# Performance work log

Hardware: AMD Instinct MI355X
Metric: run time of the kernel (lower is better)

Reference implementation:

```python
import jax, jax.numpy as jnp
import numpy as np

BUCKETS = 256


def _gru_cell(x, h, W_ih, W_hh, b_ih, b_hh):
    # torch GRUCell math, gate order (r, z, n)
    gi = x @ W_ih.T + b_ih            # [B, 3H]
    gh = h @ W_hh.T + b_hh            # [B, 3H]
    i_r, i_z, i_n = jnp.split(gi, 3, axis=-1)
    h_r, h_z, h_n = jnp.split(gh, 3, axis=-1)
    r = jax.nn.sigmoid(i_r + h_r)
    z = jax.nn.sigmoid(i_z + h_z)
    n = jnp.tanh(i_n + r * h_n)
    return (1.0 - z) * n + z * h


def setup_inputs() -> dict:
    key = jax.random.key(0)
    ks = jax.random.split(key, 10)
    B, T, C, G, H, V = 16, 2000, 128, 512, 512, BUCKETS
    s = 0.1  # keep gates in a sane range
    return {
        "cond": jax.random.normal(ks[0], (B, T, C), jnp.float32),
        "h0": jnp.zeros((B, G), jnp.float32),
        "W_ih": jax.random.normal(ks[1], (3 * G, C), jnp.float32) * s,
        "W_hh": jax.random.normal(ks[2], (3 * G, G), jnp.float32) * s,
        "b_ih": jax.random.normal(ks[3], (3 * G,), jnp.float32) * s,
        "b_hh": jax.random.normal(ks[4], (3 * G,), jnp.float32) * s,
        "W_hid": jax.random.normal(ks[5], (H, G), jnp.float32) * s,
        "b_hid": jax.random.normal(ks[6], (H,), jnp.float32) * s,
        "W_out": jax.random.normal(ks[7], (V, H), jnp.float32) * s,
        "b_out": jax.random.normal(ks[8], (V,), jnp.float32) * s,
        "embedding": jax.random.normal(ks[9], (V, C), jnp.float32) * s,
    }


def reference(cond, h0, W_ih, W_hh, b_ih, b_hh, W_hid, b_hid, W_out, b_out, embedding):
    B, T, C = cond.shape
    keys = jax.random.split(jax.random.key(1), T)
    prev0 = jnp.full((B,), BUCKETS // 2, jnp.int32)  # mid-bucket = mu-law zero

    def step(carry, inp):
        h, prev = carry
        cond_t, k = inp
        x = cond_t + embedding[prev]                  # [B, C]
        h = _gru_cell(x, h, W_ih, W_hh, b_ih, b_hh)   # [B, G]
        hid = jax.nn.relu(h @ W_hid.T + b_hid)        # [B, H]
        logits = hid @ W_out.T + b_out                # [B, V]
        sample = jax.random.categorical(k, logits, axis=-1).astype(jnp.int32)
        return (h, sample), (logits, sample)

    (h_final, _), (logits, samples) = jax.lax.scan(
        step, (h0, prev0), (jnp.swapaxes(cond, 0, 1), keys))
    # logits: [T, B, V] -> [B, T, V]; samples: [T, B] -> [B, T]
    return jnp.swapaxes(logits, 0, 1), jnp.swapaxes(samples, 0, 1), h_final
```

## Files before the change

### kernel.cpp

```cpp
#include <hip/hip_runtime.h>
#include <stdint.h>
#include <math.h>

#define NBLK 128
#define NTHR 256
#define Bn 16
#define Tn 2000
#define Cn 128
#define Gn 512
#define Hn 512
#define Vn 256

#define WS_DBL_BASE 512
#define GRP_STRIDE  3072

#define OUT_SAMP ((size_t)Bn*Tn*Vn)
#define OUT_HF   (OUT_SAMP + (size_t)Bn*Tn)

__device__ __forceinline__ unsigned rotl32(unsigned v, int n) {
  return (v << n) | (v >> (32 - n));
}

__device__ __forceinline__ void threefry2x32(unsigned k0, unsigned k1,
                                             unsigned c0, unsigned c1,
                                             unsigned& o0, unsigned& o1) {
  unsigned ks2 = k0 ^ k1 ^ 0x1BD11BDAu;
  unsigned x0 = c0 + k0;
  unsigned x1 = c1 + k1;
#define TF_R(r) { x0 += x1; x1 = rotl32(x1, r); x1 ^= x0; }
  TF_R(13) TF_R(15) TF_R(26) TF_R(6)
  x0 += k1;  x1 += ks2 + 1u;
  TF_R(17) TF_R(29) TF_R(16) TF_R(24)
  x0 += ks2; x1 += k0 + 2u;
  TF_R(13) TF_R(15) TF_R(26) TF_R(6)
  x0 += k0;  x1 += k1 + 3u;
  TF_R(17) TF_R(29) TF_R(16) TF_R(24)
  x0 += k1;  x1 += ks2 + 4u;
  TF_R(13) TF_R(15) TF_R(26) TF_R(6)
  x0 += ks2; x1 += k0 + 5u;
#undef TF_R
  o0 = x0; o1 = x1;
}

__device__ __forceinline__ void st_bypass(double* p, double v) {
  __hip_atomic_store(p, v, __ATOMIC_RELAXED, __HIP_MEMORY_SCOPE_AGENT);
}
__device__ __forceinline__ double ld_bypass(const double* p) {
  return __hip_atomic_load(p, __ATOMIC_RELAXED, __HIP_MEMORY_SCOPE_AGENT);
}

__device__ __forceinline__ void gbar8(unsigned* flags, int slot, unsigned target) {
  asm volatile("s_waitcnt vmcnt(0)" ::: "memory");
  __syncthreads();
  if (threadIdx.x == 0)
    __hip_atomic_store(&flags[slot], target, __ATOMIC_RELAXED,
                       __HIP_MEMORY_SCOPE_AGENT);
  if (threadIdx.x < 8) {
    int guard = 0;
    while (__hip_atomic_load(&flags[threadIdx.x], __ATOMIC_RELAXED,
                             __HIP_MEMORY_SCOPE_AGENT) < target) {
      if (++guard > 5000000) break;
    }
  }
  asm volatile("" ::: "memory");
  __syncthreads();
}

extern "C" __global__ __launch_bounds__(NTHR)
void wavernn_groups(const float* __restrict__ cond, const float* __restrict__ h0,
                    const float* __restrict__ W_ih, const float* __restrict__ W_hh,
                    const float* __restrict__ b_ih, const float* __restrict__ b_hh,
                    const float* __restrict__ W_hid, const float* __restrict__ b_hid,
                    const float* __restrict__ W_out, const float* __restrict__ b_out,
                    const float* __restrict__ emb,
                    float* __restrict__ out, double* __restrict__ ws) {
  const int tid = threadIdx.x;
  const int blk = blockIdx.x;
  const int g = blk >> 3;
  const int j = blk & 7;

  unsigned* flags = ((unsigned*)ws) + (size_t)g * 64;
  double* G   = ws + WS_DBL_BASE + (size_t)g * GRP_STRIDE;
  double* Hb0 = G;
  double* Hb1 = G + 512;
  double* PL  = G + 1024;

  __shared__ __attribute__((aligned(32))) double s_x[Cn];
  __shared__ __attribute__((aligned(32))) double s_h[Gn];
  __shared__ __attribute__((aligned(32))) double s_hid[64];
  __shared__ double s_r[64], s_z[64], s_hn[64], s_in[64];
  __shared__ double s_part[64][4];
  __shared__ double s_red[NTHR];
  __shared__ int    s_idx[NTHR];

  if (tid < 64) st_bypass(&Hb0[j * 64 + tid],
                          (double)h0[(size_t)g * Gn + j * 64 + tid]);
  if (tid < Cn) s_x[tid] = (double)cond[(size_t)g * Tn * Cn + tid]
                         + (double)emb[128 * Cn + tid];
  unsigned pc = 1;
  gbar8(flags, j, pc++);

  for (int t = 0; t < Tn; ++t) {
    double* hcur = (t & 1) ? Hb1 : Hb0;
    double* hnxt = (t & 1) ? Hb0 : Hb1;

    s_h[tid] = ld_bypass(&hcur[tid]);
    s_h[tid + 256] = ld_bypass(&hcur[tid + 256]);
    __syncthreads();
    {
      const int part = tid >> 6, gl = tid & 63;
      const double4* x4 = (const double4*)s_x;
      const double4* h4 = (const double4*)s_h;
      if (part <= 1) {
        const int row = part * 512 + j * 64 + gl;
        const float4* wi = (const float4*)(W_ih + (size_t)row * Cn);
        const float4* wh = (const float4*)(W_hh + (size_t)row * Gn);
        double a0 = 0., a1 = 0., a2 = 0., a3 = 0.;
#pragma unroll 8
        for (int k = 0; k < Cn / 4; ++k) {
          float4 w = wi[k]; double4 xv = x4[k];
          a0 = fma((double)w.x, xv.x, a0); a1 = fma((double)w.y, xv.y, a1);
          a2 = fma((double)w.z, xv.z, a2); a3 = fma((double)w.w, xv.w, a3);
        }
#pragma unroll 8
        for (int k = 0; k < Gn / 4; ++k) {
          float4 w = wh[k]; double4 hv = h4[k];
          a0 = fma((double)w.x, hv.x, a0); a1 = fma((double)w.y, hv.y, a1);
          a2 = fma((double)w.z, hv.z, a2); a3 = fma((double)w.w, hv.w, a3);
        }
        double pre = ((a0 + a1) + (a2 + a3)) + (double)b_ih[row] + (double)b_hh[row];
        double sig = 1.0 / (1.0 + exp(-pre));
        if (part == 0) s_r[gl] = sig; else s_z[gl] = sig;
      } else if (part == 2) {
        const int row = 1024 + j * 64 + gl;
        const float4* wh = (const float4*)(W_hh + (size_t)row * Gn);
        double a0 = 0., a1 = 0., a2 = 0., a3 = 0.;
#pragma unroll 8
        for (int k = 0; k < Gn / 4; ++k) {
          float4 w = wh[k]; double4 hv = h4[k];
          a0 = fma((double)w.x, hv.x, a0); a1 = fma((double)w.y, hv.y, a1);
          a2 = fma((double)w.z, hv.z, a2); a3 = fma((double)w.w, hv.w, a3);
        }
        s_hn[gl] = ((a0 + a1) + (a2 + a3)) + (double)b_hh[row];
      } else {
        const int row = 1024 + j * 64 + gl;
        const float4* wi = (const float4*)(W_ih + (size_t)row * Cn);
        double a0 = 0., a1 = 0., a2 = 0., a3 = 0.;
#pragma unroll 8
        for (int k = 0; k < Cn / 4; ++k) {
          float4 w = wi[k]; double4 xv = x4[k];
          a0 = fma((double)w.x, xv.x, a0); a1 = fma((double)w.y, xv.y, a1);
          a2 = fma((double)w.z, xv.z, a2); a3 = fma((double)w.w, xv.w, a3);
        }
        s_in[gl] = ((a0 + a1) + (a2 + a3)) + (double)b_ih[row];
      }
    }
    __syncthreads();
    if (tid < 64) {
      double r = s_r[tid], z = s_z[tid];
      double n = tanh(s_in[tid] + r * s_hn[tid]);
      double hv = (1.0 - z) * n + z * s_h[j * 64 + tid];
      st_bypass(&hnxt[j * 64 + tid], hv);
    }
    gbar8(flags, j, pc++);

    float cond_next = 0.f;
    if (t + 1 < Tn && tid < Cn)
      cond_next = cond[((size_t)g * Tn + (t + 1)) * Cn + tid];

    s_h[tid] = ld_bypass(&hnxt[tid]);
    s_h[tid + 256] = ld_bypass(&hnxt[tid + 256]);
    __syncthreads();
    if (t == Tn - 1 && j == 0) {
      out[OUT_HF + (size_t)g * Gn + tid] = (float)s_h[tid];
      out[OUT_HF + (size_t)g * Gn + tid + 256] = (float)s_h[tid + 256];
    }
    {
      const int row = j * 64 + (tid >> 2);
      const int q = tid & 3;
      const float4* wr = (const float4*)(W_hid + (size_t)row * Gn + q * 128);
      const double4* hh = (const double4*)(s_h + q * 128);
      double a0 = 0., a1 = 0., a2 = 0., a3 = 0.;
#pragma unroll 8
      for (int k = 0; k < 32; ++k) {
        float4 w = wr[k]; double4 hv = hh[k];
        a0 = fma((double)w.x, hv.x, a0); a1 = fma((double)w.y, hv.y, a1);
        a2 = fma((double)w.z, hv.z, a2); a3 = fma((double)w.w, hv.w, a3);
      }
      s_part[tid >> 2][q] = (a0 + a1) + (a2 + a3);
    }
    __syncthreads();
    if (tid < 64) {
      double acc = (s_part[tid][0] + s_part[tid][1])
                 + (s_part[tid][2] + s_part[tid][3])
                 + (double)b_hid[j * 64 + tid];
      s_hid[tid] = acc > 0.0 ? acc : 0.0;
    }
    __syncthreads();
    {
      const int v = tid;
      const float4* wr = (const float4*)(W_out + (size_t)v * Hn + j * 64);
      const double4* hh = (const double4*)s_hid;
      double a0 = 0., a1 = 0., a2 = 0., a3 = 0.;
#pragma unroll 8
      for (int k = 0; k < 16; ++k) {
        float4 w = wr[k]; double4 hv = hh[k];
        a0 = fma((double)w.x, hv.x, a0); a1 = fma((double)w.y, hv.y, a1);
        a2 = fma((double)w.z, hv.z, a2); a3 = fma((double)w.w, hv.w, a3);
      }
      st_bypass(&PL[j * 256 + v], (a0 + a1) + (a2 + a3));
    }
    gbar8(flags, j, pc++);

    {
      const int v = tid;
      double l0 = ld_bypass(&PL[0 * 256 + v]);
      double l1 = ld_bypass(&PL[1 * 256 + v]);
      double l2 = ld_bypass(&PL[2 * 256 + v]);
      double l3 = ld_bypass(&PL[3 * 256 + v]);
      double l4 = ld_bypass(&PL[4 * 256 + v]);
      double l5 = ld_bypass(&PL[5 * 256 + v]);
      double l6 = ld_bypass(&PL[6 * 256 + v]);
      double l7 = ld_bypass(&PL[7 * 256 + v]);
      double logit = ((((((((l0 + l1) + l2) + l3) + l4) + l5) + l6) + l7))
                   + (double)b_out[v];
      if (j == 0)
        out[(size_t)g * Tn * Vn + (size_t)t * Vn + v] = (float)logit;

      unsigned kt0, kt1, r0, r1;
      threefry2x32(0u, 1u, 0u, (unsigned)t, kt0, kt1);
      threefry2x32(kt0, kt1, 0u, (unsigned)(g * Vn + v), r0, r1);
      unsigned bits = r0 ^ r1;
      float uf = __uint_as_float((bits >> 9) | 0x3f800000u) - 1.0f;
      if (uf <= 0.f) uf = 1.17549435e-38f;
      double gum = -log(-log((double)uf));
      s_red[tid] = logit + gum;
      s_idx[tid] = v;
    }
    __syncthreads();
    for (int s2 = NTHR / 2; s2 > 0; s2 >>= 1) {
      if (tid < s2) {
        double ov = s_red[tid + s2]; int oi = s_idx[tid + s2];
        if (ov > s_red[tid] || (ov == s_red[tid] && oi < s_idx[tid])) {
          s_red[tid] = ov; s_idx[tid] = oi;
        }
      }
      __syncthreads();
    }
    const int samp = s_idx[0];
    if (tid == 0 && j == 0) out[OUT_SAMP + (size_t)g * Tn + t] = (float)samp;
    if (t + 1 < Tn && tid < Cn) {
      s_x[tid] = (double)cond_next + (double)emb[(size_t)samp * Cn + tid];
    }
  }
}

extern "C" void kernel_launch(void* const* d_in, const int* in_sizes, int n_in,
                              void* d_out, int out_size, void* d_ws, size_t ws_size,
                              hipStream_t stream) {
  const float* cond  = (const float*)d_in[0];
  const float* h0    = (const float*)d_in[1];
  const float* W_ih  = (const float*)d_in[2];
  const float* W_hh  = (const float*)d_in[3];
  const float* b_ih  = (const float*)d_in[4];
  const float* b_hh  = (const float*)d_in[5];
  const float* W_hid = (const float*)d_in[6];
  const float* b_hid = (const float*)d_in[7];
  const float* W_out = (const float*)d_in[8];
  const float* b_out = (const float*)d_in[9];
  const float* emb   = (const float*)d_in[10];

  hipMemsetAsync(d_ws, 0, 4096, stream);
  hipLaunchKernelGGL(wavernn_groups, dim3(NBLK), dim3(NTHR), 0, stream,
                     cond, h0, W_ih, W_hh, b_ih, b_hh, W_hid, b_hid,
                     W_out, b_out, emb, (float*)d_out, (double*)d_ws);
}
```

Measured before the change: 55.52 ms.

## Split group barrier into arrive/wait, overlap RNG, use wave-shuffle argmax

The group barrier is split into an arrive phase and a wait phase. The Threefry key derivation and the Gumbel noise computation now run between them, so they overlap with waiting on the other blocks. Atomic relaxed loads and stores are replaced by inline-asm global loads and stores with sc0/sc1 cache-bypass bits, using vectorised dwordx4 hidden-state loads and a batched 8-way partial-logit load. The 8-round shared-memory argmax tree becomes a 64-lane xor-shuffle reduction plus a 4-wave combine, and the W_hid partial-sum mapping is transposed. The hand-written asm depends on the correct cache-coherence bits for cross-block visibility.

```diff
diff --git a/kernel.cpp b/kernel.cpp
--- a/kernel.cpp
+++ b/kernel.cpp
@@ -16,6 +16,8 @@
 
 #define OUT_SAMP ((size_t)Bn*Tn*Vn)
 #define OUT_HF   (OUT_SAMP + (size_t)Bn*Tn)
+
+typedef __attribute__((ext_vector_type(2))) double d2_t;
 
 __device__ __forceinline__ unsigned rotl32(unsigned v, int n) {
   return (v << n) | (v >> (32 - n));
@@ -42,23 +44,57 @@
   o0 = x0; o1 = x1;
 }
 
-__device__ __forceinline__ void st_bypass(double* p, double v) {
-  __hip_atomic_store(p, v, __ATOMIC_RELAXED, __HIP_MEMORY_SCOPE_AGENT);
-}
-__device__ __forceinline__ double ld_bypass(const double* p) {
-  return __hip_atomic_load(p, __ATOMIC_RELAXED, __HIP_MEMORY_SCOPE_AGENT);
-}
-
-__device__ __forceinline__ void gbar8(unsigned* flags, int slot, unsigned target) {
+__device__ __forceinline__ void st_d(double* p, double v) {
+  asm volatile("global_store_dwordx2 %0, %1, off sc0 sc1"
+               :: "v"(p), "v"(v) : "memory");
+}
+__device__ __forceinline__ d2_t ld_d2(const double* p) {
+  d2_t r;
+  asm volatile("global_load_dwordx4 %0, %1, off sc0 sc1\n\t"
+               "s_waitcnt vmcnt(0)" : "=v"(r) : "v"(p));
+  return r;
+}
+__device__ __forceinline__ void ld8(const double* pl, int v, double* o) {
+  const double* a0 = pl + v;
+  const double* a1 = pl + 512 + v;
+  const double* a2 = pl + 1024 + v;
+  const double* a3 = pl + 1536 + v;
+  double o0, o1, o2, o3, o4, o5, o6, o7;
+  asm volatile(
+    "global_load_dwordx2 %[r0], %[p0], off sc0 sc1\n\t"
+    "global_load_dwordx2 %[r1], %[p0], off offset:2048 sc0 sc1\n\t"
+    "global_load_dwordx2 %[r2], %[p1], off sc0 sc1\n\t"
+    "global_load_dwordx2 %[r3], %[p1], off offset:2048 sc0 sc1\n\t"
+    "global_load_dwordx2 %[r4], %[p2], off sc0 sc1\n\t"
+    "global_load_dwordx2 %[r5], %[p2], off offset:2048 sc0 sc1\n\t"
+    "global_load_dwordx2 %[r6], %[p3], off sc0 sc1\n\t"
+    "global_load_dwordx2 %[r7], %[p3], off offset:2048 sc0 sc1\n\t"
+    "s_waitcnt vmcnt(0)"
+    : [r0]"=v"(o0), [r1]"=v"(o1), [r2]"=v"(o2), [r3]"=v"(o3),
+      [r4]"=v"(o4), [r5]"=v"(o5), [r6]"=v"(o6), [r7]"=v"(o7)
+    : [p0]"v"(a0), [p1]"v"(a1), [p2]"v"(a2), [p3]"v"(a3));
+  o[0]=o0; o[1]=o1; o[2]=o2; o[3]=o3; o[4]=o4; o[5]=o5; o[6]=o6; o[7]=o7;
+}
+__device__ __forceinline__ unsigned ld_u(const unsigned* p) {
+  unsigned r;
+  asm volatile("global_load_dword %0, %1, off sc0 sc1\n\t"
+               "s_waitcnt vmcnt(0)" : "=v"(r) : "v"(p) : "memory");
+  return r;
+}
+__device__ __forceinline__ void st_u(unsigned* p, unsigned v) {
+  asm volatile("global_store_dword %0, %1, off sc0 sc1"
+               :: "v"(p), "v"(v) : "memory");
+}
+
+__device__ __forceinline__ void gar(unsigned* flags, int slot, unsigned target) {
   asm volatile("s_waitcnt vmcnt(0)" ::: "memory");
   __syncthreads();
-  if (threadIdx.x == 0)
-    __hip_atomic_store(&flags[slot], target, __ATOMIC_RELAXED,
-                       __HIP_MEMORY_SCOPE_AGENT);
+  if (threadIdx.x == 0) st_u(&flags[slot], target);
+}
+__device__ __forceinline__ void gwt(unsigned* flags, unsigned target) {
   if (threadIdx.x < 8) {
     int guard = 0;
-    while (__hip_atomic_load(&flags[threadIdx.x], __ATOMIC_RELAXED,
-                             __HIP_MEMORY_SCOPE_AGENT) < target) {
+    while (ld_u(&flags[threadIdx.x]) < target) {
       if (++guard > 5000000) break;
     }
   }
@@ -89,23 +125,22 @@
   __shared__ __attribute__((aligned(32))) double s_h[Gn];
   __shared__ __attribute__((aligned(32))) double s_hid[64];
   __shared__ double s_r[64], s_z[64], s_hn[64], s_in[64];
-  __shared__ double s_part[64][4];
-  __shared__ double s_red[NTHR];
-  __shared__ int    s_idx[NTHR];
-
-  if (tid < 64) st_bypass(&Hb0[j * 64 + tid],
-                          (double)h0[(size_t)g * Gn + j * 64 + tid]);
+  __shared__ double s_part[4][64];
+  __shared__ double s_pv[4];
+  __shared__ int    s_pi[4];
+
+  if (tid < 64) st_d(&Hb0[j * 64 + tid],
+                     (double)h0[(size_t)g * Gn + j * 64 + tid]);
   if (tid < Cn) s_x[tid] = (double)cond[(size_t)g * Tn * Cn + tid]
                          + (double)emb[128 * Cn + tid];
   unsigned pc = 1;
-  gbar8(flags, j, pc++);
+  gar(flags, j, pc); gwt(flags, pc); pc++;
 
   for (int t = 0; t < Tn; ++t) {
     double* hcur = (t & 1) ? Hb1 : Hb0;
     double* hnxt = (t & 1) ? Hb0 : Hb1;
 
-    s_h[tid] = ld_bypass(&hcur[tid]);
-    s_h[tid + 256] = ld_bypass(&hcur[tid + 256]);
+    ((d2_t*)s_h)[tid] = ld_d2(hcur + 2 * tid);
     __syncthreads();
     {
       const int part = tid >> 6, gl = tid & 63;
@@ -160,24 +195,25 @@
       double r = s_r[tid], z = s_z[tid];
       double n = tanh(s_in[tid] + r * s_hn[tid]);
       double hv = (1.0 - z) * n + z * s_h[j * 64 + tid];
-      st_bypass(&hnxt[j * 64 + tid], hv);
-    }
-    gbar8(flags, j, pc++);
-
+      st_d(&hnxt[j * 64 + tid], hv);
+    }
+    gar(flags, j, pc);
     float cond_next = 0.f;
     if (t + 1 < Tn && tid < Cn)
       cond_next = cond[((size_t)g * Tn + (t + 1)) * Cn + tid];
-
-    s_h[tid] = ld_bypass(&hnxt[tid]);
-    s_h[tid + 256] = ld_bypass(&hnxt[tid + 256]);
+    unsigned kt0, kt1;
+    threefry2x32(0u, 1u, 0u, (unsigned)t, kt0, kt1);
+    gwt(flags, pc); pc++;
+
+    ((d2_t*)s_h)[tid] = ld_d2(hnxt + 2 * tid);
     __syncthreads();
     if (t == Tn - 1 && j == 0) {
       out[OUT_HF + (size_t)g * Gn + tid] = (float)s_h[tid];
       out[OUT_HF + (size_t)g * Gn + tid + 256] = (float)s_h[tid + 256];
     }
     {
-      const int row = j * 64 + (tid >> 2);
-      const int q = tid & 3;
+      const int row = j * 64 + (tid & 63);
+      const int q = tid >> 6;
       const float4* wr = (const float4*)(W_hid + (size_t)row * Gn + q * 128);
       const double4* hh = (const double4*)(s_h + q * 128);
       double a0 = 0., a1 = 0., a2 = 0., a3 = 0.;
@@ -187,12 +223,12 @@
         a0 = fma((double)w.x, hv.x, a0); a1 = fma((double)w.y, hv.y, a1);
         a2 = fma((double)w.z, hv.z, a2); a3 = fma((double)w.w, hv.w, a3);
       }
-      s_part[tid >> 2][q] = (a0 + a1) + (a2 + a3);
+      s_part[q][tid & 63] = (a0 + a1) + (a2 + a3);
     }
     __syncthreads();
     if (tid < 64) {
-      double acc = (s_part[tid][0] + s_part[tid][1])
-                 + (s_part[tid][2] + s_part[tid][3])
+      double acc = (s_part[0][tid] + s_part[1][tid])
+                 + (s_part[2][tid] + s_part[3][tid])
                  + (double)b_hid[j * 64 + tid];
       s_hid[tid] = acc > 0.0 ? acc : 0.0;
     }
@@ -208,46 +244,48 @@
         a0 = fma((double)w.x, hv.x, a0); a1 = fma((double)w.y, hv.y, a1);
         a2 = fma((double)w.z, hv.z, a2); a3 = fma((double)w.w, hv.w, a3);
       }
-      st_bypass(&PL[j * 256 + v], (a0 + a1) + (a2 + a3));
-    }
-    gbar8(flags, j, pc++);
-
-    {
-      const int v = tid;
-      double l0 = ld_bypass(&PL[0 * 256 + v]);
-      double l1 = ld_bypass(&PL[1 * 256 + v]);
-      double l2 = ld_bypass(&PL[2 * 256 + v]);
-      double l3 = ld_bypass(&PL[3 * 256 + v]);
-      double l4 = ld_bypass(&PL[4 * 256 + v]);
-      double l5 = ld_bypass(&PL[5 * 256 + v]);
-      double l6 = ld_bypass(&PL[6 * 256 + v]);
-      double l7 = ld_bypass(&PL[7 * 256 + v]);
-      double logit = ((((((((l0 + l1) + l2) + l3) + l4) + l5) + l6) + l7))
-                   + (double)b_out[v];
-      if (j == 0)
-        out[(size_t)g * Tn * Vn + (size_t)t * Vn + v] = (float)logit;
-
-      unsigned kt0, kt1, r0, r1;
-      threefry2x32(0u, 1u, 0u, (unsigned)t, kt0, kt1);
-      threefry2x32(kt0, kt1, 0u, (unsigned)(g * Vn + v), r0, r1);
+      st_d(&PL[j * 256 + v], (a0 + a1) + (a2 + a3));
+    }
+    gar(flags, j, pc);
+    double gum;
+    {
+      unsigned r0, r1;
+      threefry2x32(kt0, kt1, 0u, (unsigned)(g * Vn + tid), r0, r1);
       unsigned bits = r0 ^ r1;
       float uf = __uint_as_float((bits >> 9) | 0x3f800000u) - 1.0f;
       if (uf <= 0.f) uf = 1.17549435e-38f;
-      double gum = -log(-log((double)uf));
-      s_red[tid] = logit + gum;
-      s_idx[tid] = v;
-    }
-    __syncthreads();
-    for (int s2 = NTHR / 2; s2 > 0; s2 >>= 1) {
-      if (tid < s2) {
-        double ov = s_red[tid + s2]; int oi = s_idx[tid + s2];
-        if (ov > s_red[tid] || (ov == s_red[tid] && oi < s_idx[tid])) {
-          s_red[tid] = ov; s_idx[tid] = oi;
-        }
-      }
+      gum = -log(-log((double)uf));
+    }
+    gwt(flags, pc); pc++;
+
+    int samp;
+    {
+      const int v = tid;
+      double l[8];
+      ld8(PL, v, l);
+      double logit = ((((((((l[0] + l[1]) + l[2]) + l[3]) + l[4]) + l[5])
+                       + l[6]) + l[7])) + (double)b_out[v];
+      if (j == 0)
+        out[(size_t)g * Tn * Vn + (size_t)t * Vn + v] = (float)logit;
+
+      double bv = logit + gum;
+      int bi = v;
+#pragma unroll
+      for (int off = 1; off < 64; off <<= 1) {
+        double ov = __shfl_xor(bv, off, 64);
+        int oi = __shfl_xor(bi, off, 64);
+        if (ov > bv || (ov == bv && oi < bi)) { bv = ov; bi = oi; }
+      }
+      if ((tid & 63) == 0) { s_pv[tid >> 6] = bv; s_pi[tid >> 6] = bi; }
       __syncthreads();
-    }
-    const int samp = s_idx[0];
+      double fv = s_pv[0]; int fi = s_pi[0];
+#pragma unroll
+      for (int w = 1; w < 4; ++w) {
+        double ov = s_pv[w]; int oi = s_pi[w];
+        if (ov > fv || (ov == fv && oi < fi)) { fv = ov; fi = oi; }
+      }
+      samp = fi;
+    }
     if (tid == 0 && j == 0) out[OUT_SAMP + (size_t)g * Tn + t] = (float)samp;
     if (t + 1 < Tn && tid < Cn) {
       s_x[tid] = (double)cond_next + (double)emb[(size_t)samp * Cn + tid];
```

Result: faster. 51.33 ms (-7.5%).
